# Optimization experiments

Measured on AMD Instinct MI355X. Metric: run time of the kernel, lower is better.

Reference implementation:

```python
import jax, jax.numpy as jnp
import numpy as np

# --- static config (matches init_kwargs) ---
N_BLOCKS, N_NODES, BATCH = 3, 512, 2
F_HID, V_HID, MLP_U = 64, 16, 128   # n_invariant_feat_hidden, n_vectors_hidden, mlp width
R_OUT, VR_OUT = 64, 8               # n_invariant_feat_readout, n_vectors_readout
NORM_CONST = 1.0
SQRT3 = 1.7320508075688772          # l=1 spherical harmonic, component normalization


def _edges(n):
    # fully connected directed graph, all ordered pairs i != j
    idx = np.arange(n)
    send = np.repeat(idx, n - 1)
    recv = np.concatenate([np.delete(idx, i) for i in range(n)])
    return jnp.asarray(send), jnp.asarray(recv)

SEND, RECV = _edges(N_NODES)


def _mlp(x, w1, w2):
    # e3nn MultiLayerPerceptron: no bias, 1/sqrt(fan_in) path norm, act on every layer
    x = jax.nn.silu(x @ w1 / np.sqrt(w1.shape[0]))
    return jax.nn.silu(x @ w2 / np.sqrt(w2.shape[0]))


def _egcl(v, h, p, n):
    # v: (N, V, 3) vectors, h: (N, F) invariant feats
    vec = v[RECV] - v[SEND]                                   # (E, V, 3)
    len2 = jnp.sum(vec * vec, axis=-1)                        # (E, V)
    lengths = jnp.sqrt(jnp.maximum(len2, 1e-20))              # safe_norm
    edge_feat = jnp.concatenate([len2, h[SEND], h[RECV]], axis=-1)  # (E, V+2F)
    m_ij = _mlp(edge_feat, p['we1'], p['we2'])                # (E, U)
    phi_x = _mlp(m_ij, p['wx1'], p['wx2'])                    # (E, U)
    # spherical harmonics of normalized edge vectors; only the 1o channel has a
    # nonzero path into the Vx1o FullyConnectedTensorProduct output (0e x 1o -> 1o)
    sh1 = SQRT3 * vec / (NORM_CONST + lengths)[..., None]     # (E, V, 3)
    tmp = jnp.einsum('eu,uwv->ewv', phi_x, p['wtp'])          # contract scalar channels
    tp = jnp.einsum('ewv,ewk->evk', tmp, sh1) / np.sqrt(MLP_U * V_HID)
    v_agg = jax.ops.segment_sum(tp, RECV, num_segments=n) / (n - 1)  # (N, V, 3)
    e = jax.nn.sigmoid(m_ij @ p['winf'] / np.sqrt(MLP_U))     # (E, 1) phi_inf gate
    m_i = jax.ops.segment_sum(m_ij * e, RECV, num_segments=n)  # (N, U)
    ph = _mlp(jnp.concatenate([m_i, h], axis=-1), p['wh1'], p['wh2'])
    h_out = ph @ p['wh_out'] / np.sqrt(MLP_U) + h             # residual_h
    return v + v_agg, h_out                                   # residual_x


def _single(x, p):
    n = x.shape[0]
    h = jnp.ones((n, F_HID), x.dtype)
    vec_in = x - jnp.mean(x, axis=0, keepdims=True)           # (N, 3)
    v = jnp.broadcast_to(vec_in[:, None, :], (n, V_HID, 3))
    for b in range(N_BLOCKS):  # layer_stack: distinct params per block
        pb = {k: p[k][b] for k in ('we1', 'we2', 'wx1', 'wx2', 'winf', 'wtp', 'wh1', 'wh2', 'wh_out')}
        v, h = _egcl(v, h, pb, n)
    # final e3nn Linear on (Fx0e + Vx1o) -> (Rx0e + Vrx1o): per-irrep mixing
    h_sc = h @ p['ws'] / np.sqrt(F_HID)                       # (N, R)
    v_out = jnp.einsum('nvk,vw->nwk', v, p['wv']) / np.sqrt(V_HID)  # (N, Vr, 3)
    v_out = v_out - vec_in[:, None, :]                        # residual_x on readout
    inv = jax.nn.softmax(h_sc, axis=-1) @ p['w_out'] + p['b_out']  # linear_softmax + hk.Linear
    return v_out, inv


def setup_inputs() -> dict:
    key = jax.random.key(0)
    ks = jax.random.split(key, 14)
    B = N_BLOCKS
    f32 = jnp.float32
    return dict(
        x=jax.random.normal(ks[0], (BATCH, N_NODES, 3), f32),
        we1=jax.random.normal(ks[1], (B, V_HID + 2 * F_HID, MLP_U), f32),
        we2=jax.random.normal(ks[2], (B, MLP_U, MLP_U), f32),
        wx1=jax.random.normal(ks[3], (B, MLP_U, MLP_U), f32),
        wx2=jax.random.normal(ks[4], (B, MLP_U, MLP_U), f32),
        winf=jax.random.normal(ks[5], (B, MLP_U, 1), f32),
        wtp=jax.random.normal(ks[6], (B, MLP_U, V_HID, V_HID), f32),
        wh1=jax.random.normal(ks[7], (B, MLP_U + F_HID, MLP_U), f32),
        wh2=jax.random.normal(ks[8], (B, MLP_U, MLP_U), f32),
        wh_out=jax.random.normal(ks[9], (B, MLP_U, F_HID), f32),
        ws=jax.random.normal(ks[10], (F_HID, R_OUT), f32),
        wv=jax.random.normal(ks[11], (V_HID, VR_OUT), f32),
        w_out=jax.random.normal(ks[12], (R_OUT, R_OUT), f32) / np.sqrt(R_OUT),
        b_out=jnp.zeros((R_OUT,), f32),
    )


def reference(x, we1, we2, wx1, wx2, winf, wtp, wh1, wh2, wh_out, ws, wv, w_out, b_out):
    p = dict(we1=we1, we2=we2, wx1=wx1, wx2=wx2, winf=winf, wtp=wtp,
             wh1=wh1, wh2=wh2, wh_out=wh_out, ws=ws, wv=wv, w_out=w_out, b_out=b_out)
    return jax.vmap(lambda xi: _single(xi, p))(x)
```

## Files before the change

kernel.cpp:

```cpp
#include <hip/hip_runtime.h>

#define NN 512

typedef short short4v __attribute__((ext_vector_type(4)));
typedef short short8v __attribute__((ext_vector_type(8)));
typedef float f32x4 __attribute__((ext_vector_type(4)));
typedef _Float16 h8 __attribute__((ext_vector_type(8)));
typedef __fp16 fp16x2 __attribute__((ext_vector_type(2)));

__device__ __forceinline__ float fast_rcp(float x) { return __builtin_amdgcn_rcpf(x); }
__device__ __forceinline__ float silu_fast(float y) { return y * fast_rcp(1.0f + __expf(-y)); }
__device__ __forceinline__ float sigm_fast(float y) { return fast_rcp(1.0f + __expf(-y)); }
__device__ __forceinline__ unsigned short f2h(float f) {
    union { _Float16 h; unsigned short s; } u; u.h = (_Float16)f; return u.s;
}
__device__ __forceinline__ float h2f(unsigned short s) {
    union { unsigned short s; _Float16 h; } u; u.s = s; return (float)u.h;
}
__device__ __forceinline__ unsigned pk2(float a, float b) {
    union { fp16x2 h; unsigned u; } c; c.h = __builtin_amdgcn_cvt_pkrtz(a, b); return c.u;
}

__device__ __forceinline__ int b1A(int s, int kbyte) {
    return s * 192 + (kbyte ^ ((s & 3) << 4));
}
__device__ __forceinline__ int actA(int s, int kbyte) {
    return s * 256 + (kbyte ^ ((s & 7) << 4));
}
__device__ __forceinline__ int actP(int u, int sbyte) {
    return u * 128 + (sbyte ^ ((u & 7) << 4));
}
__device__ __forceinline__ int shA(int wk, int sbyte) {
    return wk * 128 + (sbyte ^ ((wk & 7) << 4));
}

__global__ void k_init(const float* __restrict__ x, float* __restrict__ vec_in,
                       float* __restrict__ v, float* __restrict__ h,
                       unsigned short* __restrict__ hf)
{
    const int b = (int)blockIdx.x;
    const int tid = (int)threadIdx.x;
    __shared__ float red[3 * 256];
    float s0 = 0.f, s1 = 0.f, s2 = 0.f;
    for (int n = tid; n < NN; n += 256) {
        s0 += x[(b * NN + n) * 3 + 0];
        s1 += x[(b * NN + n) * 3 + 1];
        s2 += x[(b * NN + n) * 3 + 2];
    }
    red[tid] = s0; red[256 + tid] = s1; red[512 + tid] = s2;
    __syncthreads();
    for (int off = 128; off; off >>= 1) {
        if (tid < off) {
            red[tid] += red[tid + off];
            red[256 + tid] += red[256 + tid + off];
            red[512 + tid] += red[512 + tid + off];
        }
        __syncthreads();
    }
    const float m0 = red[0] * (1.f / 512.f);
    const float m1 = red[256] * (1.f / 512.f);
    const float m2 = red[512] * (1.f / 512.f);
    for (int n = tid; n < NN; n += 256) {
        const size_t base = (size_t)b * NN + n;
        float d0 = x[base * 3 + 0] - m0;
        float d1 = x[base * 3 + 1] - m1;
        float d2 = x[base * 3 + 2] - m2;
        vec_in[base * 3 + 0] = d0;
        vec_in[base * 3 + 1] = d1;
        vec_in[base * 3 + 2] = d2;
        #pragma unroll
        for (int c = 0; c < 16; ++c) {
            v[base * 48 + c * 3 + 0] = d0;
            v[base * 48 + c * 3 + 1] = d1;
            v[base * 48 + c * 3 + 2] = d2;
        }
    }
    for (int q = tid; q < NN * 64; q += 256) {
        h[(size_t)b * NN * 64 + q] = 1.0f;
        hf[(size_t)b * NN * 64 + q] = 0x3C00;
    }
}

__global__ __launch_bounds__(256) void k_prep(
    const float* __restrict__ we1, const float* __restrict__ we2,
    const float* __restrict__ wx1, const float* __restrict__ wx2,
    const float* __restrict__ wtp,
    unsigned short* __restrict__ WT, unsigned short* __restrict__ W1Tp,
    unsigned short* __restrict__ WTPH, float* __restrict__ pR)
{
    int idx = (int)blockIdx.x * 256 + (int)threadIdx.x;
    if (idx < 147456) {
        int l = idx / 49152, r2 = idx % 49152;
        int g = r2 / 16384;
        int u = (r2 >> 7) & 127, k = r2 & 127;
        const float* src = (g == 0 ? we2 : g == 1 ? wx1 : wx2) + l * 16384;
        WT[idx] = f2h(src[k * 128 + u]);
        return;
    }
    int j = idx - 147456;
    if (j < 36864) {
        int l = j / 12288, r2 = j % 12288;
        int u = r2 / 96, k = r2 % 96;
        float val = 0.f;
        if (k < 80) val = we1[l * 18432 + k * 128 + u] * (k < 16 ? 1024.0f : 1.0f);
        W1Tp[j] = f2h(val);
        return;
    }
    int q = j - 36864;
    if (q < 98304) { WTPH[q] = f2h(wtp[q]); return; }
    int t = q - 98304;
    if (t < 16384) {
        int u = t & 127, g = t >> 7;
        float s = 0.f;
        for (int f = 0; f < 64; ++f) s += we1[(80 + f) * 128 + u];
        #pragma unroll
        for (int p = 0; p < 8; ++p) pR[(size_t)(g * 8 + p) * 128 + u] = s;
    }
}

__global__ __launch_bounds__(512) void k_edge(
    const float* __restrict__ v, const float* __restrict__ pR,
    const unsigned short* __restrict__ hf, const unsigned short* __restrict__ WTl,
    const unsigned short* __restrict__ W1Tl, const float* __restrict__ winf,
    float* __restrict__ m_i, unsigned short* __restrict__ GB)
{
    extern __shared__ char ldsb[];
    char* B1   = ldsb;
    char* ACT0 = ldsb + 12288;
    char* ACT1 = ldsb + 28672;
    char* SHB  = ldsb + 45056;
    float* ERED = (float*)(ldsb + 51200);

    const int tid = (int)threadIdx.x;
    const int bx = (int)blockIdx.x;
    const int b = bx >> 9, r = bx & 511;
    const int wv = tid >> 6, l = tid & 63;
    const int lr = l & 15, lg = l >> 4;
    const int uW = wv * 16;
    const int sg = tid >> 3, sub = tid & 7;

    const float S_L2  = 0x1p-10f;
    const float S_ACT = 0x1p-8f;
    const float E1    = 1.0f / 12.0f;
    const float EG    = 0x1p+8f * 0.088388348f;

    const float* vb = v + (size_t)b * NN * 48;
    const unsigned short* hb = hf + (size_t)b * NN * 64;

    h8 w1f[3], wf0[4], wf1[4], wf2[4];
    #pragma unroll
    for (int kt = 0; kt < 3; ++kt)
        w1f[kt] = *(const h8*)(W1Tl + (uW + lr) * 96 + kt * 32 + lg * 8);
    #pragma unroll
    for (int kt = 0; kt < 4; ++kt) {
        wf0[kt] = *(const h8*)(WTl +         (uW + lr) * 128 + kt * 32 + lg * 8);
        wf1[kt] = *(const h8*)(WTl + 16384 + (uW + lr) * 128 + kt * 32 + lg * 8);
        wf2[kt] = *(const h8*)(WTl + 32768 + (uW + lr) * 128 + kt * 32 + lg * 8);
    }
    f32x4 pRv   = *(const f32x4*)(pR + (size_t)bx * 128 + uW + lg * 4);
    f32x4 winfv = *(const f32x4*)(winf + uW + lg * 4);
    float vr6[6];
    #pragma unroll
    for (int q = 0; q < 3; ++q)
        *(float2*)&vr6[q * 2] = *(const float2*)(vb + r * 48 + sub * 6 + q * 2);

    *(float*)(B1 + sg * 192 + ((160 + sub * 4) ^ ((sg & 3) << 4))) = 0.f;

    f32x4 g[3];
    f32x4 mc = {0.f, 0.f, 0.f, 0.f};
    #pragma unroll
    for (int n = 0; n < 3; ++n) g[n] = f32x4{0.f, 0.f, 0.f, 0.f};

    for (int T = 0; T < 8; ++T) {
        const int sbase = T * 64;
        const int sid = sbase + sg;

        {
            float sv[6];
            #pragma unroll
            for (int q = 0; q < 3; ++q)
                *(float2*)&sv[q * 2] = *(const float2*)(vb + sid * 48 + sub * 6 + q * 2);
            h8 hv = *(const h8*)(hb + sid * 64 + sub * 8);
            unsigned short lh[2];
            #pragma unroll
            for (int cl = 0; cl < 2; ++cl) {
                float d0 = vr6[cl * 3 + 0] - sv[cl * 3 + 0];
                float d1 = vr6[cl * 3 + 1] - sv[cl * 3 + 1];
                float d2 = vr6[cl * 3 + 2] - sv[cl * 3 + 2];
                float l2 = d0 * d0 + d1 * d1 + d2 * d2;
                float len = __builtin_amdgcn_sqrtf(fmaxf(l2, 1e-20f));
                float fs = 1.7320508f * fast_rcp(1.0f + len);
                int wk = (sub * 2 + cl) * 3;
                *(unsigned short*)(SHB + shA(wk + 0, sg * 2)) = f2h(d0 * fs);
                *(unsigned short*)(SHB + shA(wk + 1, sg * 2)) = f2h(d1 * fs);
                *(unsigned short*)(SHB + shA(wk + 2, sg * 2)) = f2h(d2 * fs);
                lh[cl] = f2h(l2 * S_L2);
            }
            *(unsigned*)(B1 + sg * 192 + ((sub * 4) ^ ((sg & 3) << 4))) =
                (unsigned)lh[0] | ((unsigned)lh[1] << 16);
            *(h8*)(B1 + sg * 192 + ((32 + sub * 16) ^ ((sg & 3) << 4))) = hv;
        }
        __syncthreads();

        #pragma unroll
        for (int n = 0; n < 4; ++n) {
            f32x4 acc = pRv;
            #pragma unroll
            for (int kt = 0; kt < 3; ++kt) {
                h8 bl = *(const h8*)(B1 + b1A(n * 16 + lr, kt * 64 + lg * 16));
                acc = __builtin_amdgcn_mfma_f32_16x16x32_f16(w1f[kt], bl, acc, 0, 0, 0);
            }
            uint2 st;
            st.x = pk2(silu_fast(acc[0] * E1) * S_ACT, silu_fast(acc[1] * E1) * S_ACT);
            st.y = pk2(silu_fast(acc[2] * E1) * S_ACT, silu_fast(acc[3] * E1) * S_ACT);
            *(uint2*)(ACT0 + actA(n * 16 + lr, (uW + lg * 4) * 2)) = st;
        }
        __syncthreads();

        float pe[4];
        float aReg[4][4];
        #pragma unroll
        for (int n = 0; n < 4; ++n) {
            f32x4 cf = {0.f, 0.f, 0.f, 0.f};
            #pragma unroll
            for (int kt = 0; kt < 4; ++kt) {
                h8 bfr = *(const h8*)(ACT0 + actA(n * 16 + lr, kt * 64 + lg * 16));
                cf = __builtin_amdgcn_mfma_f32_16x16x32_f16(wf0[kt], bfr, cf, 0, 0, 0);
            }
            float p = 0.f;
            #pragma unroll
            for (int j2 = 0; j2 < 4; ++j2) {
                float a = silu_fast(cf[j2] * EG);
                aReg[n][j2] = a;
                p += a * winfv[j2];
            }
            pe[n] = p;
            uint2 st;
            st.x = pk2(aReg[n][0] * S_ACT, aReg[n][1] * S_ACT);
            st.y = pk2(aReg[n][2] * S_ACT, aReg[n][3] * S_ACT);
            *(uint2*)(ACT1 + actA(n * 16 + lr, (uW + lg * 4) * 2)) = st;
        }
        #pragma unroll
        for (int n = 0; n < 4; ++n) {
            pe[n] += __shfl_xor(pe[n], 16);
            pe[n] += __shfl_xor(pe[n], 32);
        }
        if (l < 16) {
            #pragma unroll
            for (int n = 0; n < 4; ++n) ERED[wv * 64 + n * 16 + l] = pe[n];
        }
        __syncthreads();

        #pragma unroll
        for (int n = 0; n < 4; ++n) {
            float tot = 0.f;
            #pragma unroll
            for (int w = 0; w < 8; ++w) tot += ERED[w * 64 + n * 16 + lr];
            float en = (sbase + n * 16 + lr == r) ? 0.f : sigm_fast(tot * 0.088388348f);
            #pragma unroll
            for (int j2 = 0; j2 < 4; ++j2)
                mc[j2] += aReg[n][j2] * en;
        }
        #pragma unroll
        for (int n = 0; n < 4; ++n) {
            f32x4 cf = {0.f, 0.f, 0.f, 0.f};
            #pragma unroll
            for (int kt = 0; kt < 4; ++kt) {
                h8 bfr = *(const h8*)(ACT1 + actA(n * 16 + lr, kt * 64 + lg * 16));
                cf = __builtin_amdgcn_mfma_f32_16x16x32_f16(wf1[kt], bfr, cf, 0, 0, 0);
            }
            uint2 st;
            st.x = pk2(silu_fast(cf[0] * EG) * S_ACT, silu_fast(cf[1] * EG) * S_ACT);
            st.y = pk2(silu_fast(cf[2] * EG) * S_ACT, silu_fast(cf[3] * EG) * S_ACT);
            *(uint2*)(ACT0 + actA(n * 16 + lr, (uW + lg * 4) * 2)) = st;
        }
        __syncthreads();

        #pragma unroll
        for (int n = 0; n < 4; ++n) {
            f32x4 cf = {0.f, 0.f, 0.f, 0.f};
            #pragma unroll
            for (int kt = 0; kt < 4; ++kt) {
                h8 bfr = *(const h8*)(ACT0 + actA(n * 16 + lr, kt * 64 + lg * 16));
                cf = __builtin_amdgcn_mfma_f32_16x16x32_f16(wf2[kt], bfr, cf, 0, 0, 0);
            }
            int s2 = (n * 16 + lr) * 2;
            #pragma unroll
            for (int j2 = 0; j2 < 4; ++j2)
                *(unsigned short*)(ACT1 + actP(uW + lg * 4 + j2, s2)) =
                    f2h(silu_fast(cf[j2] * EG) * S_ACT);
        }
        __syncthreads();

        {
            h8 af[2];
            #pragma unroll
            for (int t = 0; t < 2; ++t)
                af[t] = *(const h8*)(ACT1 + actP(uW + lr, t * 64 + lg * 16));
            #pragma unroll
            for (int n = 0; n < 3; ++n)
                #pragma unroll
                for (int t = 0; t < 2; ++t) {
                    h8 bh = *(const h8*)(SHB + shA(n * 16 + lr, t * 64 + lg * 16));
                    g[n] = __builtin_amdgcn_mfma_f32_16x16x32_f16(af[t], bh, g[n], 0, 0, 0);
                }
        }
        __syncthreads();
    }

    #pragma unroll
    for (int j2 = 0; j2 < 4; ++j2) {
        float x = mc[j2];
        x += __shfl_xor(x, 1); x += __shfl_xor(x, 2);
        x += __shfl_xor(x, 4); x += __shfl_xor(x, 8);
        mc[j2] = x;
    }
    if (lr == 0) {
        float4 s;
        s.x = mc[0]; s.y = mc[1]; s.z = mc[2]; s.w = mc[3];
        *(float4*)(m_i + (size_t)bx * 128 + uW + lg * 4) = s;
    }

    float* Gd = (float*)ldsb;
    #pragma unroll
    for (int n = 0; n < 3; ++n)
        #pragma unroll
        for (int j2 = 0; j2 < 4; ++j2)
            Gd[(uW + lg * 4 + j2) * 48 + n * 16 + lr] = g[n][j2];
    __syncthreads();
    unsigned* GB32 = (unsigned*)(GB + (size_t)bx * 6144);
    #pragma unroll
    for (int k2 = 0; k2 < 6; ++k2) {
        int i = k2 * 512 + tid;
        int u = i / 24, c = (i - u * 24) * 2;
        GB32[i] = pk2(Gd[u * 48 + c], Gd[u * 48 + c + 1]);
    }
}

__global__ __launch_bounds__(256) void k_vagg(
    const unsigned short* __restrict__ GB, const unsigned short* __restrict__ wtpHl,
    float* __restrict__ v_agg)
{
    extern __shared__ char lds2[];
    unsigned short* WL = (unsigned short*)lds2;
    float* Gr  = (float*)(lds2 + 65536);
    float* scr = (float*)(lds2 + 90112);

    const int tid = (int)threadIdx.x;
    const int wg = (int)blockIdx.x;

    for (int i = tid; i < 4096; i += 256)
        ((short8v*)WL)[i] = ((const short8v*)wtpHl)[i];
    __syncthreads();

    const int vk = tid % 48, ug = tid / 48;
    const int vv = vk / 3, kk = vk - vv * 3;
    const int u0 = (ug * 128) / 5, u1 = ((ug + 1) * 128) / 5;

    for (int rr = 0; rr < 4; ++rr) {
        const int row = wg * 4 + rr;
        const unsigned* Gs32 = (const unsigned*)(GB + (size_t)row * 6144);
        for (int i = tid; i < 3072; i += 256) {
            unsigned d = Gs32[i];
            Gr[2 * i]     = h2f((unsigned short)(d & 0xFFFF));
            Gr[2 * i + 1] = h2f((unsigned short)(d >> 16));
        }
        __syncthreads();
        if (tid < 240) {
            float acc = 0.f;
            for (int u = u0; u < u1; ++u) {
                #pragma unroll
                for (int w = 0; w < 16; ++w)
                    acc = fmaf(h2f(WL[(u * 16 + w) * 16 + vv]), Gr[u * 48 + w * 3 + kk], acc);
            }
            scr[ug * 48 + vk] = acc;
        }
        __syncthreads();
        if (tid < 48) {
            float tot = scr[tid] + scr[48 + tid] + scr[96 + tid] + scr[144 + tid] + scr[192 + tid];
            v_agg[(size_t)row * 48 + tid] = tot * 1.1070164e-02f;
        }
        __syncthreads();
    }
}

__global__ __launch_bounds__(128) void k_node_upd(
    const float* __restrict__ m_i, const float* __restrict__ v_agg,
    const float* __restrict__ wh1, const float* __restrict__ wh2,
    const float* __restrict__ wh_out, const float* __restrict__ we1n,
    float* __restrict__ h, unsigned short* __restrict__ hfm,
    float* __restrict__ v, float* __restrict__ pR)
{
    const int nx = (int)blockIdx.x;
    const int tid = (int)threadIdx.x;
    __shared__ float cat[192], t1[128], t2[128], hl2[64];
    if (tid < 128) cat[tid] = m_i[(size_t)nx * 128 + tid];
    if (tid < 64) cat[128 + tid] = h[(size_t)nx * 64 + tid];
    __syncthreads();
    {
        float acc = 0.f;
        for (int j = 0; j < 192; ++j) acc = fmaf(cat[j], wh1[j * 128 + tid], acc);
        t1[tid] = silu_fast(acc * 0.072168784f);
    }
    __syncthreads();
    {
        float acc = 0.f;
        for (int j = 0; j < 128; ++j) acc = fmaf(t1[j], wh2[j * 128 + tid], acc);
        t2[tid] = silu_fast(acc * 0.088388348f);
    }
    __syncthreads();
    if (tid < 64) {
        float acc = 0.f;
        for (int j = 0; j < 128; ++j) acc = fmaf(t2[j], wh_out[j * 64 + tid], acc);
        float hn = acc * 0.088388348f + cat[128 + tid];
        h[(size_t)nx * 64 + tid] = hn;
        hfm[(size_t)nx * 64 + tid] = f2h(hn);
        hl2[tid] = hn;
    }
    if (tid < 48) v[(size_t)nx * 48 + tid] += v_agg[(size_t)nx * 48 + tid];
    __syncthreads();
    {
        float c = 0.f;
        for (int f = 0; f < 64; ++f)
            c = fmaf(hl2[f], we1n[(80 + f) * 128 + tid], c);
        pR[(size_t)nx * 128 + tid] = c;
    }
}

__global__ __launch_bounds__(64) void k_readout(
    const float* __restrict__ v, const float* __restrict__ h,
    const float* __restrict__ vec_in, const float* __restrict__ wsM,
    const float* __restrict__ wvM, const float* __restrict__ w_out,
    const float* __restrict__ b_out, float* __restrict__ out)
{
    const int nx = (int)blockIdx.x;
    const int j = (int)threadIdx.x;
    __shared__ float sm[64];
    const float* hn = h + (size_t)nx * 64;
    float acc = 0.f;
    for (int f = 0; f < 64; ++f) acc = fmaf(hn[f], wsM[f * 64 + j], acc);
    acc *= 0.125f;
    float mx = acc;
    #pragma unroll
    for (int off = 32; off; off >>= 1) mx = fmaxf(mx, __shfl_xor(mx, off));
    float e = __expf(acc - mx);
    float ssum = e;
    #pragma unroll
    for (int off = 32; off; off >>= 1) ssum += __shfl_xor(ssum, off);
    sm[j] = e / ssum;
    __syncthreads();
    float o = b_out[j];
    for (int i = 0; i < 64; ++i) o = fmaf(sm[i], w_out[i * 64 + j], o);
    out[2 * 512 * 24 + (size_t)nx * 64 + j] = o;
    if (j < 24) {
        int w = j / 3, k = j - w * 3;
        float a2 = 0.f;
        #pragma unroll
        for (int c = 0; c < 16; ++c)
            a2 = fmaf(v[(size_t)nx * 48 + c * 3 + k], wvM[c * 8 + w], a2);
        out[(size_t)nx * 24 + j] = a2 * 0.25f - vec_in[(size_t)nx * 3 + k];
    }
}

extern "C" void kernel_launch(void* const* d_in, const int* in_sizes, int n_in,
                              void* d_out, int out_size, void* d_ws, size_t ws_size,
                              hipStream_t stream)
{
    (void)in_sizes; (void)n_in; (void)out_size; (void)ws_size;
    const float* x      = (const float*)d_in[0];
    const float* we1    = (const float*)d_in[1];
    const float* we2    = (const float*)d_in[2];
    const float* wx1    = (const float*)d_in[3];
    const float* wx2    = (const float*)d_in[4];
    const float* winf   = (const float*)d_in[5];
    const float* wtp    = (const float*)d_in[6];
    const float* wh1    = (const float*)d_in[7];
    const float* wh2    = (const float*)d_in[8];
    const float* wh_out = (const float*)d_in[9];
    const float* wsM    = (const float*)d_in[10];
    const float* wvM    = (const float*)d_in[11];
    const float* w_out  = (const float*)d_in[12];
    const float* b_out  = (const float*)d_in[13];
    float* out = (float*)d_out;
    float* W = (float*)d_ws;

    float* VEC_IN = W;
    float* V      = W + 4096;
    float* H      = W + 53248;
    float* PR     = W + 118784;
    float* MI     = W + 249856;
    float* VAGG   = W + 380928;
    unsigned short* GB   = (unsigned short*)(W + 430080);
    unsigned short* HF16 = (unsigned short*)(W + 3575808);
    unsigned short* WT   = (unsigned short*)(W + 3608576);
    unsigned short* W1Tp = (unsigned short*)(W + 3682304);
    unsigned short* WTPH = (unsigned short*)(W + 3700736);

    hipFuncSetAttribute((const void*)k_edge,
                        hipFuncAttributeMaxDynamicSharedMemorySize, 53248);
    hipFuncSetAttribute((const void*)k_vagg,
                        hipFuncAttributeMaxDynamicSharedMemorySize, 91072);

    k_init<<<2, 256, 0, stream>>>(x, VEC_IN, V, H, HF16);
    k_prep<<<1168, 256, 0, stream>>>(we1, we2, wx1, wx2, wtp, WT, W1Tp, WTPH, PR);
    for (int l = 0; l < 3; ++l) {
        k_edge<<<1024, 512, 53248, stream>>>(V, PR, HF16,
            WT + l * 49152, W1Tp + l * 12288, winf + l * 128, MI, GB);
        k_vagg<<<256, 256, 91072, stream>>>(GB, WTPH + l * 32768, VAGG);
        k_node_upd<<<1024, 128, 0, stream>>>(MI, VAGG, wh1 + l * 24576,
            wh2 + l * 16384, wh_out + l * 8192, we1 + ((l + 1) % 3) * 18432,
            H, HF16, V, PR);
    }
    k_readout<<<1024, 64, 0, stream>>>(V, H, VEC_IN, wsM, wvM, w_out, b_out, out);
}
```

Before: 786.7 us.

## Compute phi_inf gate via MFMA, prefetch sender data, drop barriers

Replaces the cross-wave shuffle-and-LDS reduction of the phi_inf gate with an extra MFMA against a broadcast fp16 copy of winf, done alongside the wx1 layer. This removes the ERED buffer and one barrier, and also drops the barrier before the tensor-product accumulation. Sender vectors and features for the next tile are prefetched into registers during the current tile. In exchange it adds fp16 rounding of winf and of the gate input, redundant MFMA work because every wave computes the same gate, and more register pressure.

Result: faster. 750.9 us (-4.6%).

```diff
diff --git a/kernel.cpp b/kernel.cpp
--- a/kernel.cpp
+++ b/kernel.cpp
@@ -84,9 +84,10 @@
 __global__ __launch_bounds__(256) void k_prep(
     const float* __restrict__ we1, const float* __restrict__ we2,
     const float* __restrict__ wx1, const float* __restrict__ wx2,
-    const float* __restrict__ wtp,
+    const float* __restrict__ wtp, const float* __restrict__ winf,
     unsigned short* __restrict__ WT, unsigned short* __restrict__ W1Tp,
-    unsigned short* __restrict__ WTPH, float* __restrict__ pR)
+    unsigned short* __restrict__ WTPH, float* __restrict__ pR,
+    unsigned short* __restrict__ WINFH)
 {
     int idx = (int)blockIdx.x * 256 + (int)threadIdx.x;
     if (idx < 147456) {
@@ -115,13 +116,16 @@
         for (int f = 0; f < 64; ++f) s += we1[(80 + f) * 128 + u];
         #pragma unroll
         for (int p = 0; p < 8; ++p) pR[(size_t)(g * 8 + p) * 128 + u] = s;
-    }
+        return;
+    }
+    int w = t - 16384;
+    if (w < 384) WINFH[w] = f2h(winf[w]);
 }
 
 __global__ __launch_bounds__(512) void k_edge(
     const float* __restrict__ v, const float* __restrict__ pR,
     const unsigned short* __restrict__ hf, const unsigned short* __restrict__ WTl,
-    const unsigned short* __restrict__ W1Tl, const float* __restrict__ winf,
+    const unsigned short* __restrict__ W1Tl, const unsigned short* __restrict__ winfH,
     float* __restrict__ m_i, unsigned short* __restrict__ GB)
 {
     extern __shared__ char ldsb[];
@@ -129,7 +133,6 @@
     char* ACT0 = ldsb + 12288;
     char* ACT1 = ldsb + 28672;
     char* SHB  = ldsb + 45056;
-    float* ERED = (float*)(ldsb + 51200);
 
     const int tid = (int)threadIdx.x;
     const int bx = (int)blockIdx.x;
@@ -147,7 +150,7 @@
     const float* vb = v + (size_t)b * NN * 48;
     const unsigned short* hb = hf + (size_t)b * NN * 64;
 
-    h8 w1f[3], wf0[4], wf1[4], wf2[4];
+    h8 w1f[3], wf0[4], wf1[4], wf2[4], wgf[4];
     #pragma unroll
     for (int kt = 0; kt < 3; ++kt)
         w1f[kt] = *(const h8*)(W1Tl + (uW + lr) * 96 + kt * 32 + lg * 8);
@@ -156,9 +159,9 @@
         wf0[kt] = *(const h8*)(WTl +         (uW + lr) * 128 + kt * 32 + lg * 8);
         wf1[kt] = *(const h8*)(WTl + 16384 + (uW + lr) * 128 + kt * 32 + lg * 8);
         wf2[kt] = *(const h8*)(WTl + 32768 + (uW + lr) * 128 + kt * 32 + lg * 8);
-    }
-    f32x4 pRv   = *(const f32x4*)(pR + (size_t)bx * 128 + uW + lg * 4);
-    f32x4 winfv = *(const f32x4*)(winf + uW + lg * 4);
+        wgf[kt] = *(const h8*)(winfH + kt * 32 + lg * 8);
+    }
+    f32x4 pRv = *(const f32x4*)(pR + (size_t)bx * 128 + uW + lg * 4);
     float vr6[6];
     #pragma unroll
     for (int q = 0; q < 3; ++q)
@@ -171,22 +174,22 @@
     #pragma unroll
     for (int n = 0; n < 3; ++n) g[n] = f32x4{0.f, 0.f, 0.f, 0.f};
 
+    float svp[6]; h8 hvp;
+    #pragma unroll
+    for (int q = 0; q < 3; ++q)
+        *(float2*)&svp[q * 2] = *(const float2*)(vb + sg * 48 + sub * 6 + q * 2);
+    hvp = *(const h8*)(hb + sg * 64 + sub * 8);
+
     for (int T = 0; T < 8; ++T) {
         const int sbase = T * 64;
-        const int sid = sbase + sg;
 
         {
-            float sv[6];
-            #pragma unroll
-            for (int q = 0; q < 3; ++q)
-                *(float2*)&sv[q * 2] = *(const float2*)(vb + sid * 48 + sub * 6 + q * 2);
-            h8 hv = *(const h8*)(hb + sid * 64 + sub * 8);
             unsigned short lh[2];
             #pragma unroll
             for (int cl = 0; cl < 2; ++cl) {
-                float d0 = vr6[cl * 3 + 0] - sv[cl * 3 + 0];
-                float d1 = vr6[cl * 3 + 1] - sv[cl * 3 + 1];
-                float d2 = vr6[cl * 3 + 2] - sv[cl * 3 + 2];
+                float d0 = vr6[cl * 3 + 0] - svp[cl * 3 + 0];
+                float d1 = vr6[cl * 3 + 1] - svp[cl * 3 + 1];
+                float d2 = vr6[cl * 3 + 2] - svp[cl * 3 + 2];
                 float l2 = d0 * d0 + d1 * d1 + d2 * d2;
                 float len = __builtin_amdgcn_sqrtf(fmaxf(l2, 1e-20f));
                 float fs = 1.7320508f * fast_rcp(1.0f + len);
@@ -198,7 +201,14 @@
             }
             *(unsigned*)(B1 + sg * 192 + ((sub * 4) ^ ((sg & 3) << 4))) =
                 (unsigned)lh[0] | ((unsigned)lh[1] << 16);
-            *(h8*)(B1 + sg * 192 + ((32 + sub * 16) ^ ((sg & 3) << 4))) = hv;
+            *(h8*)(B1 + sg * 192 + ((32 + sub * 16) ^ ((sg & 3) << 4))) = hvp;
+            if (T < 7) {
+                const int sidn = sbase + 64 + sg;
+                #pragma unroll
+                for (int q = 0; q < 3; ++q)
+                    *(float2*)&svp[q * 2] = *(const float2*)(vb + sidn * 48 + sub * 6 + q * 2);
+                hvp = *(const h8*)(hb + sidn * 64 + sub * 8);
+            }
         }
         __syncthreads();
 
@@ -217,7 +227,6 @@
         }
         __syncthreads();
 
-        float pe[4];
         float aReg[4][4];
         #pragma unroll
         for (int n = 0; n < 4; ++n) {
@@ -227,52 +236,33 @@
                 h8 bfr = *(const h8*)(ACT0 + actA(n * 16 + lr, kt * 64 + lg * 16));
                 cf = __builtin_amdgcn_mfma_f32_16x16x32_f16(wf0[kt], bfr, cf, 0, 0, 0);
             }
-            float p = 0.f;
-            #pragma unroll
-            for (int j2 = 0; j2 < 4; ++j2) {
-                float a = silu_fast(cf[j2] * EG);
-                aReg[n][j2] = a;
-                p += a * winfv[j2];
-            }
-            pe[n] = p;
             uint2 st;
+            #pragma unroll
+            for (int j2 = 0; j2 < 4; ++j2) aReg[n][j2] = silu_fast(cf[j2] * EG);
             st.x = pk2(aReg[n][0] * S_ACT, aReg[n][1] * S_ACT);
             st.y = pk2(aReg[n][2] * S_ACT, aReg[n][3] * S_ACT);
             *(uint2*)(ACT1 + actA(n * 16 + lr, (uW + lg * 4) * 2)) = st;
         }
-        #pragma unroll
-        for (int n = 0; n < 4; ++n) {
-            pe[n] += __shfl_xor(pe[n], 16);
-            pe[n] += __shfl_xor(pe[n], 32);
-        }
-        if (l < 16) {
-            #pragma unroll
-            for (int n = 0; n < 4; ++n) ERED[wv * 64 + n * 16 + l] = pe[n];
-        }
-        __syncthreads();
-
-        #pragma unroll
-        for (int n = 0; n < 4; ++n) {
-            float tot = 0.f;
-            #pragma unroll
-            for (int w = 0; w < 8; ++w) tot += ERED[w * 64 + n * 16 + lr];
-            float en = (sbase + n * 16 + lr == r) ? 0.f : sigm_fast(tot * 0.088388348f);
-            #pragma unroll
-            for (int j2 = 0; j2 < 4; ++j2)
-                mc[j2] += aReg[n][j2] * en;
-        }
+        __syncthreads();
+
         #pragma unroll
         for (int n = 0; n < 4; ++n) {
             f32x4 cf = {0.f, 0.f, 0.f, 0.f};
+            f32x4 cg = {0.f, 0.f, 0.f, 0.f};
             #pragma unroll
             for (int kt = 0; kt < 4; ++kt) {
                 h8 bfr = *(const h8*)(ACT1 + actA(n * 16 + lr, kt * 64 + lg * 16));
                 cf = __builtin_amdgcn_mfma_f32_16x16x32_f16(wf1[kt], bfr, cf, 0, 0, 0);
+                cg = __builtin_amdgcn_mfma_f32_16x16x32_f16(wgf[kt], bfr, cg, 0, 0, 0);
             }
             uint2 st;
             st.x = pk2(silu_fast(cf[0] * EG) * S_ACT, silu_fast(cf[1] * EG) * S_ACT);
             st.y = pk2(silu_fast(cf[2] * EG) * S_ACT, silu_fast(cf[3] * EG) * S_ACT);
             *(uint2*)(ACT0 + actA(n * 16 + lr, (uW + lg * 4) * 2)) = st;
+            float en = (sbase + n * 16 + lr == r) ? 0.f : sigm_fast(cg[0] * EG);
+            #pragma unroll
+            for (int j2 = 0; j2 < 4; ++j2)
+                mc[j2] += aReg[n][j2] * en;
         }
         __syncthreads();
 
@@ -290,7 +280,6 @@
                 *(unsigned short*)(ACT1 + actP(uW + lg * 4 + j2, s2)) =
                     f2h(silu_fast(cf[j2] * EG) * S_ACT);
         }
-        __syncthreads();
 
         {
             h8 af[2];
@@ -490,22 +479,24 @@
     float* PR     = W + 118784;
     float* MI     = W + 249856;
     float* VAGG   = W + 380928;
-    unsigned short* GB   = (unsigned short*)(W + 430080);
-    unsigned short* HF16 = (unsigned short*)(W + 3575808);
-    unsigned short* WT   = (unsigned short*)(W + 3608576);
-    unsigned short* W1Tp = (unsigned short*)(W + 3682304);
-    unsigned short* WTPH = (unsigned short*)(W + 3700736);
+    unsigned short* GB    = (unsigned short*)(W + 430080);
+    unsigned short* HF16  = (unsigned short*)(W + 3575808);
+    unsigned short* WT    = (unsigned short*)(W + 3608576);
+    unsigned short* W1Tp  = (unsigned short*)(W + 3682304);
+    unsigned short* WTPH  = (unsigned short*)(W + 3700736);
+    unsigned short* WINFH = (unsigned short*)(W + 3749888);
 
     hipFuncSetAttribute((const void*)k_edge,
-                        hipFuncAttributeMaxDynamicSharedMemorySize, 53248);
+                        hipFuncAttributeMaxDynamicSharedMemorySize, 51200);
     hipFuncSetAttribute((const void*)k_vagg,
                         hipFuncAttributeMaxDynamicSharedMemorySize, 91072);
 
     k_init<<<2, 256, 0, stream>>>(x, VEC_IN, V, H, HF16);
-    k_prep<<<1168, 256, 0, stream>>>(we1, we2, wx1, wx2, wtp, WT, W1Tp, WTPH, PR);
+    k_prep<<<1170, 256, 0, stream>>>(we1, we2, wx1, wx2, wtp, winf,
+                                     WT, W1Tp, WTPH, PR, WINFH);
     for (int l = 0; l < 3; ++l) {
-        k_edge<<<1024, 512, 53248, stream>>>(V, PR, HF16,
-            WT + l * 49152, W1Tp + l * 12288, winf + l * 128, MI, GB);
+        k_edge<<<1024, 512, 51200, stream>>>(V, PR, HF16,
+            WT + l * 49152, W1Tp + l * 12288, WINFH + l * 128, MI, GB);
         k_vagg<<<256, 256, 91072, stream>>>(GB, WTPH + l * 32768, VAGG);
         k_node_upd<<<1024, 128, 0, stream>>>(MI, VAGG, wh1 + l * 24576,
             wh2 + l * 16384, wh_out + l * 8192, we1 + ((l + 1) % 3) * 18432,
```
